# Kernel optimization log

Measured on AMD Instinct MI355X. Metric: run time of the kernel, lower is better.

Reference implementation:

```python
import jax, jax.numpy as jnp
import numpy as np

B, T, H, D = 2, 1024, 8, 64
C = H * D            # 512 = n_embd = heads*head_dim
M = 32768            # external memory size
TOPK = 32
SCALE = D ** -0.5
EPS_NORM = 1e-12


def _layernorm(x, w, b, eps=1e-5):
    mu = jnp.mean(x, axis=-1, keepdims=True)
    var = jnp.var(x, axis=-1, keepdims=True)
    return (x - mu) * jax.lax.rsqrt(var + eps) * w + b


def _l2norm(x):
    n = jnp.linalg.norm(x, axis=-1, keepdims=True)
    return x / jnp.maximum(n, EPS_NORM)


def setup_inputs() -> dict:
    key = jax.random.key(0)
    ks = jax.random.split(key, 12)
    s = C ** -0.5
    return {
        "x": jax.random.normal(ks[0], (B, T, C), jnp.float32),
        "memory_kv": jax.random.normal(ks[1], (B, M, 2, C), jnp.float32),
        "ln_w": jnp.ones((C,), jnp.float32),
        "ln_b": jnp.zeros((C,), jnp.float32),
        "Wq": jax.random.normal(ks[2], (C, C), jnp.float32) * s,
        "bq": jnp.zeros((C,), jnp.float32),
        "Wk": jax.random.normal(ks[3], (C, C), jnp.float32) * s,
        "bk": jnp.zeros((C,), jnp.float32),
        "Wv": jax.random.normal(ks[4], (C, C), jnp.float32) * s,
        "bv": jnp.zeros((C,), jnp.float32),
        "Wo": jax.random.normal(ks[5], (C, C), jnp.float32) * s,
        "bo": jnp.zeros((C,), jnp.float32),
        "gate_bias": jax.random.normal(ks[6], (H, 1, 1), jnp.float32),
    }


def reference(x, memory_kv, ln_w, ln_b, Wq, bq, Wk, bk, Wv, bv, Wo, bo, gate_bias):
    xn = _layernorm(x, ln_w, ln_b)
    q = _l2norm(xn @ Wq + bq)           # [B,T,C], F.normalize(dim=-1)
    k = _l2norm(xn @ Wk + bk)
    v = xn @ Wv + bv

    qh = q.reshape(B, T, H, D).transpose(0, 2, 1, 3)   # b h t d
    kh = k.reshape(B, T, H, D).transpose(0, 2, 1, 3)
    vh = v.reshape(B, T, H, D).transpose(0, 2, 1, 3)

    # local causal attention
    qk = jnp.einsum('bhid,bhjd->bhij', qh, kh) * SCALE
    causal = jnp.triu(jnp.ones((T, T), bool), k=1)
    qk = jnp.where(causal, -jnp.inf, qk)
    attn = jax.nn.softmax(qk, axis=-1)
    qkv = attn @ vh                                     # b h t d

    # kNN retrieval: top-k inner product of flat queries vs stored keys
    q_flat = q                                          # b t C (normalized)
    mem_keys = memory_kv[:, :, 0]                       # b M C
    scores = jnp.einsum('btc,bmc->btm', q_flat, mem_keys)
    _, idx = jax.lax.top_k(scores, TOPK)                # b t k
    # gather retrieved kv: [b, t, k, 2, C]
    mem = jnp.take_along_axis(memory_kv[:, None], idx[:, :, :, None, None], axis=2)
    mem_k = mem[..., 0, :].reshape(B, T, TOPK, H, D).transpose(0, 3, 1, 2, 4)  # b h t k d
    mem_v = mem[..., 1, :].reshape(B, T, TOPK, H, D).transpose(0, 3, 1, 2, 4)

    mem_qk = jnp.einsum('bhtd,bhtkd->bhtk', qh, mem_k) * SCALE
    mem_attn = jax.nn.softmax(mem_qk, axis=-1)
    mem_qkv = jnp.einsum('bhtk,bhtkd->bhtd', mem_attn, mem_v)

    combined = mem_qkv * gate_bias + qkv * (1.0 - gate_bias)  # gate_bias [H,1,1]
    combined = combined.transpose(0, 2, 1, 3).reshape(B, T, C)
    out = combined @ Wo + bo

    current_kv = jnp.stack((k, v), axis=-2)             # b t 2 C (normalized keys)
    return out, current_kv
```

## Files before the change

kernel.cpp:

```cpp
#include <hip/hip_runtime.h>
#include <hip/hip_bf16.h>

#define B_ 2
#define T_ 1024
#define H_ 8
#define D_ 64
#define C_ 512
#define M_ 32768
#define TOPK_ 32
#define NCAND_ 64
#define SCALE_ 0.125f
#define QSCALE_ 360.0f
#define KSCALE_ 24.0f
#define OSCALE_ 20.0f

typedef unsigned short u16;
typedef float    f32x2  __attribute__((ext_vector_type(2)));
typedef float    f32x4  __attribute__((ext_vector_type(4)));
typedef __bf16   bf16x8 __attribute__((ext_vector_type(8)));
typedef u16      u16x4  __attribute__((ext_vector_type(4)));
typedef int      i32x4  __attribute__((ext_vector_type(4)));
typedef unsigned char u8x4 __attribute__((ext_vector_type(4)));

__device__ __forceinline__ u16 f2bf(float f) {
  __hip_bfloat16 b = __float2bfloat16(f);
  u16 u; __builtin_memcpy(&u, &b, 2); return u;
}

__device__ __forceinline__ unsigned char q8(float v, float scale) {
  int iv = (int)rintf(v * scale);
  iv = iv > 127 ? 127 : (iv < -127 ? -127 : iv);
  return (unsigned char)(signed char)iv;
}

__device__ __forceinline__ void gl_lds16(const void* g, void* l) {
  __builtin_amdgcn_global_load_lds(
      (const __attribute__((address_space(1))) void*)g,
      (__attribute__((address_space(3))) void*)l, 16, 0, 0);
}

__global__ __launch_bounds__(256) void wtrans_kernel(
    const float* __restrict__ W0, const float* __restrict__ W1,
    const float* __restrict__ W2, u16* __restrict__ WT) {
  __shared__ u16 tl[32][33];
  int z = blockIdx.z;
  const float* W = (z == 0) ? W0 : (z == 1) ? W1 : W2;
  u16* dst = WT + (size_t)z * C_ * C_;
  int n0 = blockIdx.x * 32, k0 = blockIdx.y * 32;
  int tx = threadIdx.x, ty = threadIdx.y;
#pragma unroll
  for (int i = 0; i < 4; ++i) {
    int k = k0 + ty + i * 8;
    tl[ty + i * 8][tx] = f2bf(W[(size_t)k * C_ + n0 + tx]);
  }
  __syncthreads();
#pragma unroll
  for (int i = 0; i < 4; ++i) {
    int nn = ty + i * 8;
    dst[(size_t)(n0 + nn) * C_ + k0 + tx] = tl[tx][nn];
  }
}

__global__ __launch_bounds__(256) void prep_keys_kernel(
    const float* __restrict__ mem, char* __restrict__ ki) {
  const int n4 = B_ * M_ * C_ / 4;
  for (int i = blockIdx.x * 256 + threadIdx.x; i < n4; i += gridDim.x * 256) {
    int row = i >> 7;
    int c4 = i & 127;
    f32x4 v = *(const f32x4*)(mem + ((size_t)row * 1024) + c4 * 4);
    u8x4 o;
    o[0] = q8(v[0], KSCALE_); o[1] = q8(v[1], KSCALE_);
    o[2] = q8(v[2], KSCALE_); o[3] = q8(v[3], KSCALE_);
    *(u8x4*)((unsigned char*)ki + (size_t)i * 4) = o;
  }
}

__global__ __launch_bounds__(256) void ln_kernel(
    const float* __restrict__ x, const float* __restrict__ w,
    const float* __restrict__ bia, u16* __restrict__ xn, float* __restrict__ xnf) {
  int row = blockIdx.x * 4 + (threadIdx.x >> 6);
  int lane = threadIdx.x & 63;
  const float* xr = x + (size_t)row * C_;
  f32x4 v0 = *(const f32x4*)(xr + lane * 4);
  f32x4 v1 = *(const f32x4*)(xr + 256 + lane * 4);
  float s = v0[0] + v0[1] + v0[2] + v0[3] + v1[0] + v1[1] + v1[2] + v1[3];
  float q = v0[0]*v0[0]+v0[1]*v0[1]+v0[2]*v0[2]+v0[3]*v0[3]
          + v1[0]*v1[0]+v1[1]*v1[1]+v1[2]*v1[2]+v1[3]*v1[3];
#pragma unroll
  for (int m = 1; m < 64; m <<= 1) { s += __shfl_xor(s, m); q += __shfl_xor(q, m); }
  float mean = s * (1.0f / C_);
  float var  = q * (1.0f / C_) - mean * mean;
  float rs = rsqrtf(var + 1e-5f);
  u16x4 o0, o1;
  f32x4 f0, f1;
#pragma unroll
  for (int e = 0; e < 4; ++e) {
    int c = lane * 4 + e;
    f0[e] = (v0[e] - mean) * rs * w[c] + bia[c];
    o0[e] = f2bf(f0[e]);
    int c2 = 256 + lane * 4 + e;
    f1[e] = (v1[e] - mean) * rs * w[c2] + bia[c2];
    o1[e] = f2bf(f1[e]);
  }
  *(u16x4*)(xn + (size_t)row * C_ + lane * 4) = o0;
  *(u16x4*)(xn + (size_t)row * C_ + 256 + lane * 4) = o1;
  *(f32x4*)(xnf + (size_t)row * C_ + lane * 4) = f0;
  *(f32x4*)(xnf + (size_t)row * C_ + 256 + lane * 4) = f1;
}

__global__ __launch_bounds__(256) void gemm_f32(
    const float* __restrict__ A, const float* __restrict__ Bw,
    const float* __restrict__ bias, float* __restrict__ Cout) {
  __shared__ float As[64][33];
  __shared__ float Bs[32][64];
  int tid = threadIdx.x;
  int tx = tid & 15, ty = tid >> 4;
  int r0 = blockIdx.x * 64, c0 = blockIdx.y * 64;
  f32x4 acc[4];
#pragma unroll
  for (int i = 0; i < 4; ++i) acc[i] = f32x4{0.f, 0.f, 0.f, 0.f};
  for (int kt = 0; kt < 16; ++kt) {
    int k0 = kt * 32;
#pragma unroll
    for (int i2 = 0; i2 < 2; ++i2) {
      int idx = i2 * 256 + tid;
      int arow = idx >> 3, ac = idx & 7;
      f32x4 av = *(const f32x4*)(A + (size_t)(r0 + arow) * 512 + k0 + ac * 4);
      As[arow][ac * 4 + 0] = av[0]; As[arow][ac * 4 + 1] = av[1];
      As[arow][ac * 4 + 2] = av[2]; As[arow][ac * 4 + 3] = av[3];
      int krow = idx >> 4, cc = idx & 15;
      f32x4 bv = *(const f32x4*)(Bw + (size_t)(k0 + krow) * 512 + c0 + cc * 4);
      *(f32x4*)(&Bs[krow][cc * 4]) = bv;
    }
    __syncthreads();
#pragma unroll
    for (int kk = 0; kk < 32; ++kk) {
      f32x4 bv = *(const f32x4*)(&Bs[kk][tx * 4]);
#pragma unroll
      for (int i = 0; i < 4; ++i) {
        float av = As[ty * 4 + i][kk];
        acc[i] += av * bv;
      }
    }
    __syncthreads();
  }
  f32x4 bb = *(const f32x4*)(bias + c0 + tx * 4);
#pragma unroll
  for (int i = 0; i < 4; ++i)
    *(f32x4*)(Cout + (size_t)(r0 + ty * 4 + i) * 512 + c0 + tx * 4) = acc[i] + bb;
}

__global__ __launch_bounds__(256) void gemm128(
    const u16* __restrict__ A, long aBS,
    const u16* __restrict__ Bt, long bBS,
    float* __restrict__ Cf, long cBS,
    const float* __restrict__ bias, const float* __restrict__ bias2, int ldc) {
  __shared__ __align__(16) u16 As[128 * 64];
  __shared__ __align__(16) u16 Bs[128 * 64];
  const int tid = threadIdx.x;
  const int lane = tid & 63, w = tid >> 6;
  const int wm = w >> 1, wn = w & 1;
  const int z = blockIdx.z;
  const u16* Ab = A + (size_t)z * aBS + (size_t)blockIdx.x * 128 * 512;
  const u16* Bb = Bt + (size_t)z * bBS + (size_t)blockIdx.y * 128 * 512;

  f32x4 acc[4][4];
#pragma unroll
  for (int i = 0; i < 4; ++i)
#pragma unroll
    for (int j = 0; j < 4; ++j) acc[i][j] = f32x4{0.f, 0.f, 0.f, 0.f};

  for (int kt = 0; kt < 8; ++kt) {
    const u16* Akt = Ab + kt * 64;
    const u16* Bkt = Bb + kt * 64;
#pragma unroll
    for (int it = 0; it < 4; ++it) {
      int slot = it * 256 + tid;
      int rr = slot >> 3, ss = slot & 7;
      int q = ss ^ (rr & 7);
      gl_lds16(Akt + (size_t)rr * 512 + q * 8, (char*)As + slot * 16);
      gl_lds16(Bkt + (size_t)rr * 512 + q * 8, (char*)Bs + slot * 16);
    }
    __syncthreads();
#pragma unroll
    for (int kk = 0; kk < 2; ++kk) {
      bf16x8 av[4], bv[4];
#pragma unroll
      for (int i = 0; i < 4; ++i) {
        int blk = kk * 4 + (lane >> 4);
        int ra = wm * 64 + i * 16 + (lane & 15);
        av[i] = *(const bf16x8*)((const char*)As + ra * 128 + ((blk ^ (ra & 7)) << 4));
        int rb = wn * 64 + i * 16 + (lane & 15);
        bv[i] = *(const bf16x8*)((const char*)Bs + rb * 128 + ((blk ^ (rb & 7)) << 4));
      }
#pragma unroll
      for (int mi = 0; mi < 4; ++mi)
#pragma unroll
        for (int ni = 0; ni < 4; ++ni)
          acc[mi][ni] = __builtin_amdgcn_mfma_f32_16x16x32_bf16(av[mi], bv[ni], acc[mi][ni], 0, 0, 0);
    }
    __syncthreads();
  }
  const float* bi = (z == 1 && bias2) ? bias2 : bias;
  const long cbase = (long)z * cBS;
  const int rsub = (lane >> 4) * 4;
  const long row0 = (long)blockIdx.x * 128 + wm * 64;
  const int col00 = wn * 64 + (lane & 15) + (int)blockIdx.y * 128;
#pragma unroll
  for (int mi = 0; mi < 4; ++mi)
#pragma unroll
    for (int rg = 0; rg < 4; ++rg) {
      long row = row0 + mi * 16 + rsub + rg;
#pragma unroll
      for (int ni = 0; ni < 4; ++ni) {
        int col = col00 + ni * 16;
        float bb = bi ? bi[col] : 0.0f;
        Cf[cbase + row * (long)ldc + col] = acc[mi][ni][rg] + bb;
      }
    }
}

__global__ __launch_bounds__(256) void gemm_sc8(
    const char* __restrict__ A, const char* __restrict__ Bt, char* __restrict__ sc8) {
  __shared__ __align__(16) char As[128 * 64];
  __shared__ __align__(16) char Bs[128 * 64];
  const int tid = threadIdx.x;
  const int lane = tid & 63, w = tid >> 6;
  const int wm = w >> 1, wn = w & 1;
  const int p = blockIdx.x;
  const int z = p >> 11;
  const int q_ = p & 2047;
  const int r = (q_ >> 3) & 7;
  const int c = ((q_ >> 6) << 3) | (q_ & 7);
  const char* Ab = A + (size_t)z * T_ * C_ + (size_t)r * 128 * 512;
  const char* Bb = Bt + (size_t)z * M_ * C_ + (size_t)c * 128 * 512;

  i32x4 acc[4][4];
#pragma unroll
  for (int i = 0; i < 4; ++i)
#pragma unroll
    for (int j = 0; j < 4; ++j) acc[i][j] = i32x4{0, 0, 0, 0};

  for (int kt = 0; kt < 8; ++kt) {
    const char* Akt = Ab + kt * 64;
    const char* Bkt = Bb + kt * 64;
#pragma unroll
    for (int it = 0; it < 2; ++it) {
      int slot = it * 256 + tid;
      int rr = slot >> 2, cw = slot & 3;
      int ch = cw ^ (rr & 3);
      gl_lds16(Akt + (size_t)rr * 512 + ch * 16, As + slot * 16);
      gl_lds16(Bkt + (size_t)rr * 512 + ch * 16, Bs + slot * 16);
    }
    __syncthreads();
    i32x4 av[4], bv[4];
#pragma unroll
    for (int i = 0; i < 4; ++i) {
      int ra = wm * 64 + i * 16 + (lane & 15);
      av[i] = *(const i32x4*)(As + ra * 64 + (((lane >> 4) ^ (ra & 3)) << 4));
      int rb = wn * 64 + i * 16 + (lane & 15);
      bv[i] = *(const i32x4*)(Bs + rb * 64 + (((lane >> 4) ^ (rb & 3)) << 4));
    }
#pragma unroll
    for (int mi = 0; mi < 4; ++mi)
#pragma unroll
      for (int ni = 0; ni < 4; ++ni)
        acc[mi][ni] = __builtin_amdgcn_mfma_i32_16x16x64_i8(av[mi], bv[ni], acc[mi][ni], 0, 0, 0);
    __syncthreads();
  }
  const int rsub = (lane >> 4) * 4;
  const long row0 = (long)r * 128 + wm * 64;
  const int col00 = c * 128 + wn * 64 + (lane & 15);
  char* base = sc8 + (size_t)z * T_ * M_;
  const float osc = OSCALE_ / (QSCALE_ * KSCALE_);
#pragma unroll
  for (int mi = 0; mi < 4; ++mi)
#pragma unroll
    for (int rg = 0; rg < 4; ++rg) {
      long row = row0 + mi * 16 + rsub + rg;
#pragma unroll
      for (int ni = 0; ni < 4; ++ni) {
        int iv = (int)rintf((float)acc[mi][ni][rg] * osc);
        iv = iv > 127 ? 127 : (iv < -127 ? -127 : iv);
        base[row * (long)M_ + col00 + ni * 16] = (char)iv;
      }
    }
}

__global__ __launch_bounds__(256) void postproc_kernel(
    const float* __restrict__ qraw, const float* __restrict__ kraw,
    const float* __restrict__ vraw, float* __restrict__ qf,
    u16* __restrict__ qb, u16* __restrict__ kb, char* __restrict__ qi,
    float* __restrict__ kvout) {
  int row = blockIdx.x * 4 + (threadIdx.x >> 6);
  int lane = threadIdx.x & 63;
  size_t rb_ = (size_t)row * C_;
  f32x4 a0 = *(const f32x4*)(qraw + rb_ + lane * 4);
  f32x4 a1 = *(const f32x4*)(qraw + rb_ + 256 + lane * 4);
  float ss = a0[0]*a0[0]+a0[1]*a0[1]+a0[2]*a0[2]+a0[3]*a0[3]
           + a1[0]*a1[0]+a1[1]*a1[1]+a1[2]*a1[2]+a1[3]*a1[3];
#pragma unroll
  for (int m = 1; m < 64; m <<= 1) ss += __shfl_xor(ss, m);
  float rn = 1.0f / fmaxf(sqrtf(ss), 1e-12f);
  f32x4 q0 = a0 * rn, q1 = a1 * rn;
  *(f32x4*)(qf + rb_ + lane * 4) = q0;
  *(f32x4*)(qf + rb_ + 256 + lane * 4) = q1;
  u16x4 t0, t1;
#pragma unroll
  for (int e = 0; e < 4; ++e) { t0[e] = f2bf(q0[e]); t1[e] = f2bf(q1[e]); }
  *(u16x4*)(qb + rb_ + lane * 4) = t0;
  *(u16x4*)(qb + rb_ + 256 + lane * 4) = t1;
  u8x4 i0, i1;
#pragma unroll
  for (int e = 0; e < 4; ++e) { i0[e] = q8(q0[e], QSCALE_); i1[e] = q8(q1[e], QSCALE_); }
  *(u8x4*)((unsigned char*)qi + rb_ + lane * 4) = i0;
  *(u8x4*)((unsigned char*)qi + rb_ + 256 + lane * 4) = i1;
  f32x4 b0 = *(const f32x4*)(kraw + rb_ + lane * 4);
  f32x4 b1 = *(const f32x4*)(kraw + rb_ + 256 + lane * 4);
  float sk = b0[0]*b0[0]+b0[1]*b0[1]+b0[2]*b0[2]+b0[3]*b0[3]
           + b1[0]*b1[0]+b1[1]*b1[1]+b1[2]*b1[2]+b1[3]*b1[3];
#pragma unroll
  for (int m = 1; m < 64; m <<= 1) sk += __shfl_xor(sk, m);
  float rk = 1.0f / fmaxf(sqrtf(sk), 1e-12f);
  f32x4 k0 = b0 * rk, k1 = b1 * rk;
  size_t kvb = (size_t)row * (2 * C_);
  *(f32x4*)(kvout + kvb + lane * 4) = k0;
  *(f32x4*)(kvout + kvb + 256 + lane * 4) = k1;
#pragma unroll
  for (int e = 0; e < 4; ++e) { t0[e] = f2bf(k0[e]); t1[e] = f2bf(k1[e]); }
  *(u16x4*)(kb + rb_ + lane * 4) = t0;
  *(u16x4*)(kb + rb_ + 256 + lane * 4) = t1;
  f32x4 c0 = *(const f32x4*)(vraw + rb_ + lane * 4);
  f32x4 c1 = *(const f32x4*)(vraw + rb_ + 256 + lane * 4);
  *(f32x4*)(kvout + kvb + C_ + lane * 4) = c0;
  *(f32x4*)(kvout + kvb + C_ + 256 + lane * 4) = c1;
}

__global__ __launch_bounds__(256) void vtrans_kernel(
    const float* __restrict__ vraw, u16* __restrict__ vT) {
  __shared__ u16 tile[64][65];
  int tt = blockIdx.x, h = blockIdx.y, b = blockIdx.z;
  int tx = threadIdx.x, ty = threadIdx.y;
#pragma unroll
  for (int i = 0; i < 8; ++i) {
    int t = tt * 64 + ty + i * 8;
    const float* src = vraw + (size_t)(b * T_ + t) * C_ + h * 64;
    tile[ty + i * 8][tx] = f2bf(src[tx]);
    tile[ty + i * 8][tx + 32] = f2bf(src[tx + 32]);
  }
  __syncthreads();
#pragma unroll
  for (int i = 0; i < 8; ++i) {
    int d = ty + i * 8;
    u16* dst = vT + ((size_t)((b * H_ + h) * 64 + d)) * T_ + tt * 64;
    dst[tx] = tile[tx][d];
    dst[tx + 32] = tile[tx + 32][d];
  }
}

__global__ __launch_bounds__(256) void attn_kernel(
    const u16* __restrict__ qb, const u16* __restrict__ kb,
    const u16* __restrict__ vT, float* __restrict__ o) {
  __shared__ __align__(16) u16 Ks[128 * 64];
  __shared__ __align__(16) u16 Vs[64 * 128];
  __shared__ __align__(16) u16 Ps[4][16 * 128];
  int tid = threadIdx.x, lane = tid & 63, w = tid >> 6;
  int it = blockIdx.x, h = blockIdx.y, b = blockIdx.z;
  int t0 = it * 64;
  bf16x8 aq[2];
#pragma unroll
  for (int kk = 0; kk < 2; ++kk) {
    int row = t0 + w * 16 + (lane & 15);
    aq[kk] = *(const bf16x8*)(qb + (size_t)(b * T_ + row) * C_ + h * 64 + kk * 32 + (lane >> 4) * 8);
  }
  f32x4 accO[4];
  float denp[4];
#pragma unroll
  for (int j = 0; j < 4; ++j) { accO[j] = f32x4{0.f,0.f,0.f,0.f}; denp[j] = 0.f; }

  int ntiles = it / 2 + 1;
  for (int jt = 0; jt < ntiles; ++jt) {
    int j0 = jt * 128;
#pragma unroll
    for (int i2 = 0; i2 < 4; ++i2) {
      int slot = i2 * 256 + tid;
      int rr = slot >> 3, ssw = slot & 7;
      int q = ssw ^ (rr & 7);
      gl_lds16(kb + (size_t)(b * T_ + j0 + rr) * C_ + h * 64 + q * 8, (char*)Ks + slot * 16);
    }
#pragma unroll
    for (int i2 = 0; i2 < 4; ++i2) {
      int slot = i2 * 256 + tid;
      int rr = slot >> 4, ssw = slot & 15;
      int q = ssw ^ (rr & 15);
      gl_lds16(vT + ((size_t)((b * H_ + h) * 64 + rr)) * T_ + j0 + q * 8, (char*)Vs + slot * 16);
    }
    __syncthreads();
    f32x4 s[8];
#pragma unroll
    for (int ni = 0; ni < 8; ++ni) s[ni] = f32x4{0.f,0.f,0.f,0.f};
#pragma unroll
    for (int kk = 0; kk < 2; ++kk) {
      bf16x8 bk[8];
#pragma unroll
      for (int ni = 0; ni < 8; ++ni) {
        int rbi = ni * 16 + (lane & 15);
        int blk = kk * 4 + (lane >> 4);
        bk[ni] = *(const bf16x8*)((const char*)Ks + rbi * 128 + ((blk ^ (rbi & 7)) << 4));
      }
#pragma unroll
      for (int ni = 0; ni < 8; ++ni)
        s[ni] = __builtin_amdgcn_mfma_f32_16x16x32_bf16(aq[kk], bk[ni], s[ni], 0, 0, 0);
    }
#pragma unroll
    for (int ni = 0; ni < 8; ++ni)
#pragma unroll
      for (int rg = 0; rg < 4; ++rg) {
        int qrow = t0 + w * 16 + (lane >> 4) * 4 + rg;
        int kvcol = j0 + ni * 16 + (lane & 15);
        float sv = s[ni][rg] * SCALE_;
        float p = (kvcol <= qrow) ? __expf(sv) : 0.0f;
        denp[rg] += p;
        int qk = (lane >> 4) * 4 + rg;
        int kvl = ni * 16 + (lane & 15);
        int blk2 = kvl >> 3;
        *(u16*)((char*)Ps[w] + qk * 256 + ((blk2 ^ qk) << 4) + (kvl & 7) * 2) = f2bf(p);
      }
#pragma unroll
    for (int kk2 = 0; kk2 < 4; ++kk2) {
      bf16x8 ap, bvv[4];
      int blk = kk2 * 4 + (lane >> 4);
      int rq = lane & 15;
      ap = *(const bf16x8*)((const char*)Ps[w] + rq * 256 + ((blk ^ rq) << 4));
#pragma unroll
      for (int nd = 0; nd < 4; ++nd) {
        int rd = nd * 16 + (lane & 15);
        bvv[nd] = *(const bf16x8*)((const char*)Vs + rd * 256 + ((blk ^ (rd & 15)) << 4));
      }
#pragma unroll
      for (int nd = 0; nd < 4; ++nd)
        accO[nd] = __builtin_amdgcn_mfma_f32_16x16x32_bf16(ap, bvv[nd], accO[nd], 0, 0, 0);
    }
    __syncthreads();
  }
  float den[4];
#pragma unroll
  for (int rg = 0; rg < 4; ++rg) {
    float d = denp[rg];
    d += __shfl_xor(d, 1); d += __shfl_xor(d, 2);
    d += __shfl_xor(d, 4); d += __shfl_xor(d, 8);
    den[rg] = d;
  }
#pragma unroll
  for (int nd = 0; nd < 4; ++nd)
#pragma unroll
    for (int rg = 0; rg < 4; ++rg) {
      int row = t0 + w * 16 + (lane >> 4) * 4 + rg;
      int d = nd * 16 + (lane & 15);
      o[(size_t)(b * T_ + row) * C_ + h * 64 + d] = accO[nd][rg] / den[rg];
    }
}

__global__ __launch_bounds__(256) void topk_kernel(
    const char* __restrict__ scores, int* __restrict__ cand) {
  int row = blockIdx.x;
  const unsigned char* s = (const unsigned char*)scores + (size_t)row * M_;
  int tid = threadIdx.x, lane = tid & 63, w = tid >> 6;
  unsigned c[8];
#pragma unroll
  for (int i = 0; i < 8; ++i) c[i] = 0;
  for (int i2 = 0; i2 < 16; ++i2) {
    int base = i2 * 2048 + tid * 8;
    uint2 v = *(const uint2*)(s + base);
#pragma unroll
    for (int e = 0; e < 8; ++e) {
      unsigned byte = (e < 4) ? ((v.x >> (8 * e)) & 0xFF) : ((v.y >> (8 * (e - 4))) & 0xFF);
      unsigned key = byte ^ 0x80u;
      unsigned cmb = (key << 15) | (unsigned)(32767 - (base + e));
      if (cmb > c[7]) {
        c[7] = cmb;
#pragma unroll
        for (int ss = 7; ss > 0; --ss) {
          if (c[ss] > c[ss - 1]) { unsigned t = c[ss - 1]; c[ss - 1] = c[ss]; c[ss] = t; }
        }
      }
    }
  }
  __shared__ unsigned red[4];
  __shared__ unsigned winner;
  for (int r = 0; r < NCAND_; ++r) {
    unsigned bb = c[0];
#pragma unroll
    for (int m = 1; m < 64; m <<= 1) {
      unsigned o = __shfl_xor(bb, m);
      bb = (o > bb) ? o : bb;
    }
    if (lane == 0) red[w] = bb;
    __syncthreads();
    if (tid == 0) {
      unsigned m0 = red[0];
      if (red[1] > m0) m0 = red[1];
      if (red[2] > m0) m0 = red[2];
      if (red[3] > m0) m0 = red[3];
      winner = m0;
      cand[(size_t)row * NCAND_ + r] = 32767 - (int)(m0 & 32767u);
    }
    __syncthreads();
    unsigned win = winner;
    if (c[0] == win) {
#pragma unroll
      for (int ss = 0; ss < 7; ++ss) c[ss] = c[ss + 1];
      c[7] = 0;
    }
    __syncthreads();
  }
}

__global__ __launch_bounds__(256) void knn_tail_kernel(
    const float* __restrict__ qf, const float* __restrict__ mem,
    const int* __restrict__ cand, const float* __restrict__ attn,
    const float* __restrict__ gate, u16* __restrict__ comb) {
  int row = blockIdx.x, b = row >> 10;
  int tid = threadIdx.x, lane = tid & 63, w = tid >> 6;
  __shared__ float qL[512];
  __shared__ float sL[NCAND_];
  __shared__ float sHh[NCAND_][8];
  __shared__ int cL[NCAND_];
  __shared__ int wIdx[TOPK_];
  __shared__ float eL[TOPK_][8];
  qL[tid] = qf[(size_t)row * C_ + tid];
  qL[256 + tid] = qf[(size_t)row * C_ + 256 + tid];
  if (tid < NCAND_) cL[tid] = cand[(size_t)row * NCAND_ + tid];
  __syncthreads();
  for (int i = 0; i < 16; ++i) {
    int cdx = w * 16 + i;
    const float* mrow = mem + ((size_t)(b * M_ + cL[cdx])) * 1024;
    f32x4 k0 = *(const f32x4*)(mrow + lane * 8);
    f32x4 k1 = *(const f32x4*)(mrow + lane * 8 + 4);
    float p = qL[lane*8+0]*k0[0] + qL[lane*8+1]*k0[1] + qL[lane*8+2]*k0[2] + qL[lane*8+3]*k0[3]
            + qL[lane*8+4]*k1[0] + qL[lane*8+5]*k1[1] + qL[lane*8+6]*k1[2] + qL[lane*8+7]*k1[3];
    p += __shfl_xor(p, 1); p += __shfl_xor(p, 2); p += __shfl_xor(p, 4);
    if ((lane & 7) == 0) sHh[cdx][lane >> 3] = p;
    float pf = p;
    pf += __shfl_xor(pf, 8); pf += __shfl_xor(pf, 16); pf += __shfl_xor(pf, 32);
    if (lane == 0) sL[cdx] = pf;
  }
  __syncthreads();
  if (tid < NCAND_) {
    float sv = sL[tid]; int id = cL[tid];
    int rank = 0;
    for (int j = 0; j < NCAND_; ++j) {
      float sj = sL[j];
      rank += (sj > sv) || (sj == sv && cL[j] < id);
    }
    if (rank < TOPK_) {
      wIdx[rank] = id;
#pragma unroll
      for (int h = 0; h < 8; ++h)
        eL[rank][h] = __expf(sHh[tid][h] * SCALE_);
    }
  }
  __syncthreads();
  int h2 = tid >> 5, dp = tid & 31;
  float num0 = 0.f, num1 = 0.f, den = 0.f;
  for (int k = 0; k < TOPK_; ++k) {
    float wgt = eL[k][h2];
    const float* vrow = mem + ((size_t)(b * M_ + wIdx[k])) * 1024 + 512;
    f32x2 vv = *(const f32x2*)(vrow + h2 * 64 + dp * 2);
    num0 += wgt * vv[0];
    num1 += wgt * vv[1];
    den += wgt;
  }
  float g = gate[h2];
  int c0 = h2 * 64 + dp * 2;
  float a0 = attn[(size_t)row * C_ + c0];
  float a1 = attn[(size_t)row * C_ + c0 + 1];
  u16 o0 = f2bf(g * (num0 / den) + (1.0f - g) * a0);
  u16 o1 = f2bf(g * (num1 / den) + (1.0f - g) * a1);
  *(unsigned*)(comb + (size_t)row * C_ + c0) = (unsigned)o0 | ((unsigned)o1 << 16);
}

extern "C" void kernel_launch(void* const* d_in, const int* in_sizes, int n_in,
                              void* d_out, int out_size, void* d_ws, size_t ws_size,
                              hipStream_t stream) {
  const float* x    = (const float*)d_in[0];
  const float* mem  = (const float*)d_in[1];
  const float* lnw  = (const float*)d_in[2];
  const float* lnb  = (const float*)d_in[3];
  const float* Wq   = (const float*)d_in[4];
  const float* bq   = (const float*)d_in[5];
  const float* Wk   = (const float*)d_in[6];
  const float* bk   = (const float*)d_in[7];
  const float* Wv   = (const float*)d_in[8];
  const float* bv   = (const float*)d_in[9];
  const float* Wo   = (const float*)d_in[10];
  const float* bo   = (const float*)d_in[11];
  const float* gate = (const float*)d_in[12];
  float* out   = (float*)d_out;
  float* kvout = out + (size_t)B_ * T_ * C_;

  size_t off = 0;
  auto alloc = [&](size_t bytes) {
    char* r = (char*)d_ws + off;
    off += (bytes + 255) & ~(size_t)255;
    return r;
  };
  u16*      WT   = (u16*)alloc(3ull * C_ * C_ * 2);
  char*     ki   = (char*)alloc((size_t)B_ * M_ * C_);
  u16*      xn   = (u16*)alloc((size_t)B_ * T_ * C_ * 2);
  float*    xnf  = (float*)alloc((size_t)B_ * T_ * C_ * 4);
  float*    qraw = (float*)alloc((size_t)B_ * T_ * C_ * 4);
  float*    kvraw= (float*)alloc(2ull * B_ * T_ * C_ * 4);
  float*    kraw = kvraw;
  float*    vraw = kvraw + (size_t)B_ * T_ * C_;
  float*    qf   = (float*)alloc((size_t)B_ * T_ * C_ * 4);
  u16*      qb   = (u16*)alloc((size_t)B_ * T_ * C_ * 2);
  u16*      kb   = (u16*)alloc((size_t)B_ * T_ * C_ * 2);
  char*     qi   = (char*)alloc((size_t)B_ * T_ * C_);
  u16*      vT   = (u16*)alloc((size_t)B_ * T_ * C_ * 2);
  float*    attn = (float*)alloc((size_t)B_ * T_ * C_ * 4);
  char*     sc8  = (char*)alloc((size_t)B_ * T_ * M_);
  int*      candb= (int*)alloc((size_t)B_ * T_ * NCAND_ * 4);
  u16*      comb = (u16*)alloc((size_t)B_ * T_ * C_ * 2);
  if (off > ws_size) return;

  wtrans_kernel<<<dim3(16, 16, 3), dim3(32, 8), 0, stream>>>(Wk, Wv, Wo, WT);
  prep_keys_kernel<<<8192, 256, 0, stream>>>(mem, ki);
  ln_kernel<<<512, 256, 0, stream>>>(x, lnw, lnb, xn, xnf);
  gemm_f32<<<dim3(32, 8), 256, 0, stream>>>(xnf, Wq, bq, qraw);
  gemm128<<<dim3(16, 4, 2), 256, 0, stream>>>(xn, 0, WT, (long)C_ * C_,
                                              kvraw, (long)B_ * T_ * C_, bk, bv, C_);
  postproc_kernel<<<512, 256, 0, stream>>>(qraw, kraw, vraw, qf, qb, kb, qi, kvout);
  vtrans_kernel<<<dim3(16, 8, 2), dim3(32, 8), 0, stream>>>(vraw, vT);
  attn_kernel<<<dim3(16, 8, 2), 256, 0, stream>>>(qb, kb, vT, attn);
  gemm_sc8<<<4096, 256, 0, stream>>>(qi, ki, sc8);
  topk_kernel<<<2048, 256, 0, stream>>>(sc8, candb);
  knn_tail_kernel<<<2048, 256, 0, stream>>>(qf, mem, candb, attn, gate, comb);
  gemm128<<<dim3(16, 4, 1), 256, 0, stream>>>(comb, 0, WT + 2 * C_ * C_, 0,
                                              out, 0, bo, nullptr, C_);
}
```

Baseline: 348.8 us.

## Fuse top-k candidate selection into kNN tail kernel with per-wave merge

Merges the top-k candidate kernel into the kNN tail kernel, so candidate indices stay in shared memory rather than round-tripping through global memory, and one launch is removed. The 64-round block-wide selection with three barriers per round is replaced by a per-wave 64-round shuffle extraction with no barriers, followed by a rank-by-count merge over 256 wave candidates into the global top 64. It also adds unroll pragmas to the scoring loops. The cost is more shared memory and registers per block, plus a 256-wide rank loop in every thread.

After: 326.3 us. 1.07x faster.

```diff
diff --git a/kernel.cpp b/kernel.cpp
--- a/kernel.cpp
+++ b/kernel.cpp
@@ -461,67 +461,13 @@
     }
 }
 
-__global__ __launch_bounds__(256) void topk_kernel(
-    const char* __restrict__ scores, int* __restrict__ cand) {
-  int row = blockIdx.x;
-  const unsigned char* s = (const unsigned char*)scores + (size_t)row * M_;
-  int tid = threadIdx.x, lane = tid & 63, w = tid >> 6;
-  unsigned c[8];
-#pragma unroll
-  for (int i = 0; i < 8; ++i) c[i] = 0;
-  for (int i2 = 0; i2 < 16; ++i2) {
-    int base = i2 * 2048 + tid * 8;
-    uint2 v = *(const uint2*)(s + base);
-#pragma unroll
-    for (int e = 0; e < 8; ++e) {
-      unsigned byte = (e < 4) ? ((v.x >> (8 * e)) & 0xFF) : ((v.y >> (8 * (e - 4))) & 0xFF);
-      unsigned key = byte ^ 0x80u;
-      unsigned cmb = (key << 15) | (unsigned)(32767 - (base + e));
-      if (cmb > c[7]) {
-        c[7] = cmb;
-#pragma unroll
-        for (int ss = 7; ss > 0; --ss) {
-          if (c[ss] > c[ss - 1]) { unsigned t = c[ss - 1]; c[ss - 1] = c[ss]; c[ss] = t; }
-        }
-      }
-    }
-  }
-  __shared__ unsigned red[4];
-  __shared__ unsigned winner;
-  for (int r = 0; r < NCAND_; ++r) {
-    unsigned bb = c[0];
-#pragma unroll
-    for (int m = 1; m < 64; m <<= 1) {
-      unsigned o = __shfl_xor(bb, m);
-      bb = (o > bb) ? o : bb;
-    }
-    if (lane == 0) red[w] = bb;
-    __syncthreads();
-    if (tid == 0) {
-      unsigned m0 = red[0];
-      if (red[1] > m0) m0 = red[1];
-      if (red[2] > m0) m0 = red[2];
-      if (red[3] > m0) m0 = red[3];
-      winner = m0;
-      cand[(size_t)row * NCAND_ + r] = 32767 - (int)(m0 & 32767u);
-    }
-    __syncthreads();
-    unsigned win = winner;
-    if (c[0] == win) {
-#pragma unroll
-      for (int ss = 0; ss < 7; ++ss) c[ss] = c[ss + 1];
-      c[7] = 0;
-    }
-    __syncthreads();
-  }
-}
-
-__global__ __launch_bounds__(256) void knn_tail_kernel(
-    const float* __restrict__ qf, const float* __restrict__ mem,
-    const int* __restrict__ cand, const float* __restrict__ attn,
+__global__ __launch_bounds__(256) void topk_tail_kernel(
+    const char* __restrict__ scores, const float* __restrict__ qf,
+    const float* __restrict__ mem, const float* __restrict__ attn,
     const float* __restrict__ gate, u16* __restrict__ comb) {
   int row = blockIdx.x, b = row >> 10;
   int tid = threadIdx.x, lane = tid & 63, w = tid >> 6;
+  __shared__ unsigned candKey[256];
   __shared__ float qL[512];
   __shared__ float sL[NCAND_];
   __shared__ float sHh[NCAND_][8];
@@ -530,8 +476,50 @@
   __shared__ float eL[TOPK_][8];
   qL[tid] = qf[(size_t)row * C_ + tid];
   qL[256 + tid] = qf[(size_t)row * C_ + 256 + tid];
-  if (tid < NCAND_) cL[tid] = cand[(size_t)row * NCAND_ + tid];
+  const unsigned char* s = (const unsigned char*)scores + (size_t)row * M_;
+  unsigned c[8];
+#pragma unroll
+  for (int i = 0; i < 8; ++i) c[i] = 0;
+  for (int i2 = 0; i2 < 16; ++i2) {
+    int base = i2 * 2048 + tid * 8;
+    uint2 v = *(const uint2*)(s + base);
+#pragma unroll
+    for (int e = 0; e < 8; ++e) {
+      unsigned byte = (e < 4) ? ((v.x >> (8 * e)) & 0xFF) : ((v.y >> (8 * (e - 4))) & 0xFF);
+      unsigned key = byte ^ 0x80u;
+      unsigned cmb = (key << 15) | (unsigned)(32767 - (base + e));
+      if (cmb > c[7]) {
+        c[7] = cmb;
+#pragma unroll
+        for (int ss = 7; ss > 0; --ss) {
+          if (c[ss] > c[ss - 1]) { unsigned t = c[ss - 1]; c[ss - 1] = c[ss]; c[ss] = t; }
+        }
+      }
+    }
+  }
+  for (int r = 0; r < 64; ++r) {
+    unsigned bb = c[0];
+#pragma unroll
+    for (int m = 1; m < 64; m <<= 1) {
+      unsigned o = __shfl_xor(bb, m);
+      bb = (o > bb) ? o : bb;
+    }
+    if (lane == 0) candKey[w * 64 + r] = bb;
+    if (c[0] == bb) {
+#pragma unroll
+      for (int ss = 0; ss < 7; ++ss) c[ss] = c[ss + 1];
+      c[7] = 0;
+    }
+  }
   __syncthreads();
+  {
+    unsigned my = candKey[tid];
+    int rank = 0;
+    for (int j = 0; j < 256; ++j) rank += (candKey[j] > my);
+    if (rank < NCAND_) cL[rank] = 32767 - (int)(my & 32767u);
+  }
+  __syncthreads();
+#pragma unroll 4
   for (int i = 0; i < 16; ++i) {
     int cdx = w * 16 + i;
     const float* mrow = mem + ((size_t)(b * M_ + cL[cdx])) * 1024;
@@ -549,6 +537,7 @@
   if (tid < NCAND_) {
     float sv = sL[tid]; int id = cL[tid];
     int rank = 0;
+#pragma unroll
     for (int j = 0; j < NCAND_; ++j) {
       float sj = sL[j];
       rank += (sj > sv) || (sj == sv && cL[j] < id);
@@ -563,6 +552,7 @@
   __syncthreads();
   int h2 = tid >> 5, dp = tid & 31;
   float num0 = 0.f, num1 = 0.f, den = 0.f;
+#pragma unroll 8
   for (int k = 0; k < TOPK_; ++k) {
     float wgt = eL[k][h2];
     const float* vrow = mem + ((size_t)(b * M_ + wIdx[k])) * 1024 + 512;
@@ -620,7 +610,6 @@
   u16*      vT   = (u16*)alloc((size_t)B_ * T_ * C_ * 2);
   float*    attn = (float*)alloc((size_t)B_ * T_ * C_ * 4);
   char*     sc8  = (char*)alloc((size_t)B_ * T_ * M_);
-  int*      candb= (int*)alloc((size_t)B_ * T_ * NCAND_ * 4);
   u16*      comb = (u16*)alloc((size_t)B_ * T_ * C_ * 2);
   if (off > ws_size) return;
 
@@ -634,8 +623,7 @@
   vtrans_kernel<<<dim3(16, 8, 2), dim3(32, 8), 0, stream>>>(vraw, vT);
   attn_kernel<<<dim3(16, 8, 2), 256, 0, stream>>>(qb, kb, vT, attn);
   gemm_sc8<<<4096, 256, 0, stream>>>(qi, ki, sc8);
-  topk_kernel<<<2048, 256, 0, stream>>>(sc8, candb);
-  knn_tail_kernel<<<2048, 256, 0, stream>>>(qf, mem, candb, attn, gate, comb);
+  topk_tail_kernel<<<2048, 256, 0, stream>>>(sc8, qf, mem, attn, gate, comb);
   gemm128<<<dim3(16, 4, 1), 256, 0, stream>>>(comb, 0, WT + 2 * C_ * C_, 0,
                                               out, 0, bo, nullptr, C_);
 }
```
